# Kernel optimization log

Hardware: AMD Instinct MI355X
Metric: run time of the kernel (lower is better)

Reference implementation:

```python
import jax, jax.numpy as jnp
import numpy as np

D_MODEL = 1024
N_HEADS = 16
D_HEAD = 64


def setup_inputs() -> dict:
    key = jax.random.key(0)
    ks = jax.random.split(key, 5)
    B, T = 2, 2048
    scale = 1.0 / np.sqrt(D_MODEL)
    x = jax.random.normal(ks[0], (B, T, D_MODEL), dtype=jnp.float32)
    Wq = jax.random.normal(ks[1], (N_HEADS * D_HEAD, D_MODEL), dtype=jnp.float32) * scale
    Wk = jax.random.normal(ks[2], (N_HEADS * D_HEAD, D_MODEL), dtype=jnp.float32) * scale
    Wv = jax.random.normal(ks[3], (N_HEADS * D_HEAD, D_MODEL), dtype=jnp.float32) * scale
    Wo = jax.random.normal(ks[4], (D_MODEL, N_HEADS * D_HEAD), dtype=jnp.float32) * scale
    return {"x": x, "Wq": Wq, "Wk": Wk, "Wv": Wv, "Wo": Wo}


def reference(x, Wq, Wk, Wv, Wo):
    B, T, D = x.shape
    # Linear(y = x @ W.T), then split heads: [B, H, T, d]
    def split_heads(y):
        return y.reshape(B, T, N_HEADS, D_HEAD).transpose(0, 2, 1, 3)
    q = split_heads(x @ Wq.T)
    k = split_heads(x @ Wk.T)
    v = split_heads(x @ Wv.T)
    scale = D_HEAD ** -0.5
    # Materialized [B, H, T, T] scores, as in the original module
    scores = jnp.einsum('bhtd,bhTd->bhtT', q, k) * scale
    attn = jax.nn.softmax(scores, axis=-1)
    y = jnp.einsum('bhtT,bhTd->bhtd', attn, v)
    y = y.transpose(0, 2, 1, 3).reshape(B, T, N_HEADS * D_HEAD)
    return y @ Wo.T
```

## Files before the change

kernel.cpp:

```cpp
#include <hip/hip_runtime.h>
#include <hip/hip_bf16.h>

typedef __attribute__((ext_vector_type(8))) short bf16x8;
typedef __attribute__((ext_vector_type(8))) unsigned short u16x8;
typedef __attribute__((ext_vector_type(4))) float f32x4;
typedef unsigned short u16t;

#define DEVINL static __device__ __forceinline__

DEVINL u16t f2bf(float f) {
  union { __hip_bfloat16 h; u16t u; } cv;
  cv.h = __float2bfloat16(f);
  return cv.u;
}

DEVINL unsigned cvt_pk_bf16(float a, float b) {
  unsigned r;
  asm("v_cvt_pk_bf16_f32 %0, %1, %2" : "=v"(r) : "v"(a), "v"(b));
  return r;
}

DEVINL void async16(void* lds, const void* g) {
  __builtin_amdgcn_global_load_lds((const __attribute__((address_space(1))) void*)g,
                                   (__attribute__((address_space(3))) void*)lds,
                                   16, 0, 0);
}

__global__ __launch_bounds__(256) void convert_bf16(
    const float* __restrict__ x,  const float* __restrict__ wq,
    const float* __restrict__ wk, const float* __restrict__ wv,
    const float* __restrict__ wo,
    u16t* __restrict__ xb, u16t* __restrict__ wqb, u16t* __restrict__ wob) {
  const int blk = blockIdx.x;
  const int tid = threadIdx.x;
  if (blk < 896) {
    const int lane = tid & 63, w = tid >> 6;
    const int r = lane & 15, cw = lane >> 4;
    int mg, half, row0;
    const float* src; u16t* dst;
    if (blk < 512) { mg = blk >> 1; half = blk & 1; src = x; dst = xb; row0 = mg * 16; }
    else {
      const int wblk = blk - 512;
      mg = wblk >> 1; half = wblk & 1; dst = wqb;
      const int n0 = mg * 16;
      if (n0 < 1024)      { src = wq; row0 = n0; }
      else if (n0 < 2048) { src = wk; row0 = n0 - 1024; }
      else                { src = wv; row0 = n0 - 2048; }
    }
    #pragma unroll
    for (int ic = 0; ic < 4; ++ic) {
      const int c2 = half * 64 + w * 16 + ic * 4 + cw;
      const float4 v0 = *(const float4*)&src[(size_t)(row0 + r) * 1024 + c2 * 8];
      const float4 v1 = *(const float4*)&src[(size_t)(row0 + r) * 1024 + c2 * 8 + 4];
      u16x8 o;
      o[0] = f2bf(v0.x); o[1] = f2bf(v0.y); o[2] = f2bf(v0.z); o[3] = f2bf(v0.w);
      o[4] = f2bf(v1.x); o[5] = f2bf(v1.y); o[6] = f2bf(v1.z); o[7] = f2bf(v1.w);
      *(u16x8*)&dst[((size_t)mg * 128 + c2) * 128 + r * 8] = o;
    }
  } else {
    const int row = blk - 896;
    const size_t i = (size_t)row * 1024 + (size_t)tid * 4;
    const float4 v = *(const float4*)&wo[i];
    ushort4 rr;
    rr.x = f2bf(v.x); rr.y = f2bf(v.y); rr.z = f2bf(v.z); rr.w = f2bf(v.w);
    *(ushort4*)&wob[i] = rr;
  }
}

__global__ __launch_bounds__(256, 3) void gemm_fs(
    const u16t* __restrict__ A, const u16t* __restrict__ B,
    void* __restrict__ C0, void* __restrict__ C1, void* __restrict__ C2) {
  const int tid = threadIdx.x;
  const int lane = tid & 63;
  const int w = tid >> 6;
  const int wm = w >> 1, wn = w & 1;
  const int quad = lane >> 4, cl = lane & 15;
  const int m0 = blockIdx.y * 128;
  const int n0 = blockIdx.x * 128;

  const u16t* Ap = A + ((size_t)((m0 >> 4) + wm * 4) * 128 + quad) * 128 + cl * 8;
  const u16t* Bp = B + ((size_t)((n0 >> 4) + wn * 4) * 128 + quad) * 128 + cl * 8;

  f32x4 acc[4][4] = {};
  bf16x8 afA[4], bfA[4], afB[4], bfB[4];

  #define LOADP(af_, bf_, kp_)                                                \
    {                                                                         \
      _Pragma("unroll")                                                       \
      for (int i = 0; i < 4; ++i)                                             \
        af_[i] = *(const bf16x8*)&Ap[(size_t)i * 16384 + (kp_) * 512];        \
      _Pragma("unroll")                                                       \
      for (int j = 0; j < 4; ++j)                                             \
        bf_[j] = *(const bf16x8*)&Bp[(size_t)j * 16384 + (kp_) * 512];        \
    }

  #define MFMAP(af_, bf_)                                                     \
    {                                                                         \
      _Pragma("unroll")                                                       \
      for (int i = 0; i < 4; ++i)                                             \
        _Pragma("unroll")                                                     \
        for (int j = 0; j < 4; ++j)                                           \
          acc[i][j] = __builtin_amdgcn_mfma_f32_16x16x32_bf16(af_[i], bf_[j], acc[i][j], 0, 0, 0); \
    }

  LOADP(afA, bfA, 0);
  __builtin_amdgcn_sched_barrier(0);
  #pragma unroll 1
  for (int kp = 0; kp < 32; kp += 2) {
    LOADP(afB, bfB, kp + 1);
    __builtin_amdgcn_sched_barrier(0);
    MFMAP(afA, bfA);
    if (kp + 2 < 32) LOADP(afA, bfA, kp + 2);
    __builtin_amdgcn_sched_barrier(0);
    MFMAP(afB, bfB);
  }
  #undef LOADP
  #undef MFMAP

  const int nz = n0 >> 10;
  #pragma unroll
  for (int i = 0; i < 4; ++i)
    #pragma unroll
    for (int j = 0; j < 4; ++j) {
      const int mb = m0 + wm * 64 + i * 16 + quad * 4;
      const int n  = n0 + wn * 64 + j * 16 + cl;
      const int nw = n & 1023, h = nw >> 6, d = nw & 63;
      const int b = mb >> 11, tb = mb & 2047;
      const size_t bh = (size_t)(b * 16 + h);
      if (nz == 2) {
        ushort4 v4;
        v4.x = f2bf(acc[i][j][0]); v4.y = f2bf(acc[i][j][1]);
        v4.z = f2bf(acc[i][j][2]); v4.w = f2bf(acc[i][j][3]);
        const size_t addr = (bh << 17) +
            (size_t)(((d >> 4) * 256 + (tb >> 3)) * 128 + (d & 15) * 8 + (tb & 7));
        *(ushort4*)&((u16t*)C2)[addr] = v4;
      } else if (nz == 1) {
        const size_t basea = (bh << 17) +
            (size_t)(((tb >> 4) * 8 + (d >> 3)) * 128 + (d & 7));
        #pragma unroll
        for (int r = 0; r < 4; ++r)
          ((u16t*)C1)[basea + ((tb & 15) + r) * 8] = f2bf(acc[i][j][r]);
      } else {
        #pragma unroll
        for (int r = 0; r < 4; ++r)
          ((u16t*)C0)[(bh * 2048 + tb + r) * 64 + d] =
              f2bf(acc[i][j][r] * 0.18033688011112043f);
      }
    }
}

template <int MODE, int BM>
__global__ __launch_bounds__(256) void gemm_bt(
    const u16t* __restrict__ A, const u16t* __restrict__ B,
    void* __restrict__ C0, void* __restrict__ C1, void* __restrict__ C2,
    int M, int N, int K) {
  constexpr int MI = BM / 32;
  __shared__ u16t As[2][BM * 32];
  __shared__ u16t Bs[2][128 * 32];

  const int tid = threadIdx.x;
  const int lane = tid & 63;
  const int w = tid >> 6;
  const int wm = w >> 1, wn = w & 1;
  const int quad = lane >> 4, cl = lane & 15;
  const int m0 = blockIdx.y * BM;
  const int n0 = blockIdx.x * 128;

  const int srow = lane >> 2;
  const int scol = (lane & 3) * 8;

  f32x4 acc[MI][4] = {};

  #define STAGEP(b, kp)                                                       \
    {                                                                         \
      _Pragma("unroll")                                                       \
      for (int ii = 0; ii < BM / 64; ++ii) {                                  \
        const int c = w + ii * 4;                                             \
        async16(&As[b][c * 512],                                              \
                &A[(size_t)(m0 + c * 16 + srow) * K + (kp) * 32 + scol]);     \
      }                                                                       \
      _Pragma("unroll")                                                       \
      for (int ii = 0; ii < 2; ++ii) {                                        \
        const int c = w + ii * 4;                                             \
        async16(&Bs[b][c * 512],                                              \
                &B[(size_t)(n0 + c * 16 + srow) * K + (kp) * 32 + scol]);     \
      }                                                                       \
    }

  #define COMPUTEP(b)                                                         \
    {                                                                         \
      bf16x8 af[MI], bfr[4];                                                  \
      _Pragma("unroll")                                                       \
      for (int i = 0; i < MI; ++i)                                            \
        af[i] = *(const bf16x8*)&As[b][(wm * (BM / 2) + i * 16 + cl) * 32 + quad * 8]; \
      _Pragma("unroll")                                                       \
      for (int j = 0; j < 4; ++j)                                             \
        bfr[j] = *(const bf16x8*)&Bs[b][(wn * 64 + j * 16 + cl) * 32 + quad * 8]; \
      _Pragma("unroll")                                                       \
      for (int i = 0; i < MI; ++i)                                            \
        _Pragma("unroll")                                                     \
        for (int j = 0; j < 4; ++j)                                           \
          acc[i][j] = __builtin_amdgcn_mfma_f32_16x16x32_bf16(af[i], bfr[j], acc[i][j], 0, 0, 0); \
    }

  const int NP = K >> 5;
  STAGEP(0, 0);
  __syncthreads();
  for (int kp = 0; kp < NP; kp += 2) {
    if (kp + 1 < NP) STAGEP(1, kp + 1);
    COMPUTEP(0);
    __syncthreads();
    if (kp + 2 < NP) STAGEP(0, kp + 2);
    COMPUTEP(1);
    __syncthreads();
  }
  #undef STAGEP
  #undef COMPUTEP

  #pragma unroll
  for (int i = 0; i < MI; ++i)
    #pragma unroll
    for (int j = 0; j < 4; ++j) {
      const int mb = m0 + wm * (BM / 2) + i * 16 + quad * 4;
      const int n  = n0 + wn * 64 + j * 16 + cl;
      if (MODE == 0) {
        #pragma unroll
        for (int r = 0; r < 4; ++r)
          ((float*)C0)[(size_t)(mb + r) * N + n] = acc[i][j][r];
      }
      (void)C1; (void)C2;
    }
}

__global__ __launch_bounds__(256, 2) void flash_attn(
    const u16t* __restrict__ Q, const u16t* __restrict__ Kt,
    const u16t* __restrict__ Vt, u16t* __restrict__ Y) {
  __shared__ u16t Ps[4 * 32 * 136];
  const int tid = threadIdx.x;
  const int lane = tid & 63;
  const int w = tid >> 6;
  const int quad = lane >> 4, cl = lane & 15;
  const int bh = blockIdx.x;
  const int q0 = blockIdx.y * 128 + w * 32;
  const u16t* Kb = Kt + ((size_t)bh << 17);
  const u16t* Vb = Vt + ((size_t)bh << 17);

  bf16x8 aq[2][2];
  #pragma unroll
  for (int h = 0; h < 2; ++h)
    #pragma unroll
    for (int ks = 0; ks < 2; ++ks)
      aq[h][ks] = *(const bf16x8*)&Q[((size_t)bh * 2048 + q0 + 16 * h + cl) * 64 + ks * 32 + quad * 8];

  bf16x8 ones8;
  #pragma unroll
  for (int i = 0; i < 8; ++i) ones8[i] = (short)0x3F80;

  f32x4 o[2][4] = {};
  f32x4 psum[2] = {};

  u16t* Pw = &Ps[w * 32 * 136];

  for (int jt = 0; jt < 16; ++jt) {
    const int j0 = jt * 128;

    bf16x8 kf[2][8];
    #pragma unroll
    for (int ks = 0; ks < 2; ++ks)
      #pragma unroll
      for (int js = 0; js < 8; ++js)
        kf[ks][js] = *(const bf16x8*)&Kb[(size_t)((((j0 >> 4) + js) * 8 + ks * 4) * 128) + lane * 8];
    __builtin_amdgcn_sched_barrier(0);

    f32x4 s0[8] = {}, s1[8] = {};
    __builtin_amdgcn_s_setprio(1);
    #pragma unroll
    for (int ks = 0; ks < 2; ++ks) {
      #pragma unroll
      for (int js = 0; js < 8; ++js)
        s0[js] = __builtin_amdgcn_mfma_f32_16x16x32_bf16(kf[ks][js], aq[0][ks], s0[js], 0, 0, 0);
      #pragma unroll
      for (int js = 0; js < 8; ++js)
        s1[js] = __builtin_amdgcn_mfma_f32_16x16x32_bf16(kf[ks][js], aq[1][ks], s1[js], 0, 0, 0);
    }
    __builtin_amdgcn_s_setprio(0);

    bf16x8 vf[4][4];
    #pragma unroll
    for (int ks = 0; ks < 4; ++ks)
      #pragma unroll
      for (int ds = 0; ds < 4; ++ds)
        vf[ks][ds] = *(const bf16x8*)&Vb[(size_t)((ds * 256 + (j0 >> 3) + ks * 4) * 128) + lane * 8];
    __builtin_amdgcn_sched_barrier(0);

    #pragma unroll
    for (int js = 0; js < 8; ++js) {
      uint2 pk0, pk1;
      pk0.x = cvt_pk_bf16(__builtin_exp2f(s0[js][0]), __builtin_exp2f(s0[js][1]));
      pk0.y = cvt_pk_bf16(__builtin_exp2f(s0[js][2]), __builtin_exp2f(s0[js][3]));
      *(uint2*)&Pw[cl * 136 + js * 16 + quad * 4] = pk0;
      pk1.x = cvt_pk_bf16(__builtin_exp2f(s1[js][0]), __builtin_exp2f(s1[js][1]));
      pk1.y = cvt_pk_bf16(__builtin_exp2f(s1[js][2]), __builtin_exp2f(s1[js][3]));
      *(uint2*)&Pw[(16 + cl) * 136 + js * 16 + quad * 4] = pk1;
    }

    __builtin_amdgcn_s_setprio(1);
    #pragma unroll
    for (int ks = 0; ks < 4; ++ks) {
      const bf16x8 ap0 = *(const bf16x8*)&Pw[cl * 136 + ks * 32 + quad * 8];
      const bf16x8 ap1 = *(const bf16x8*)&Pw[(16 + cl) * 136 + ks * 32 + quad * 8];
      psum[0] = __builtin_amdgcn_mfma_f32_16x16x32_bf16(ap0, ones8, psum[0], 0, 0, 0);
      psum[1] = __builtin_amdgcn_mfma_f32_16x16x32_bf16(ap1, ones8, psum[1], 0, 0, 0);
      #pragma unroll
      for (int ds = 0; ds < 4; ++ds) {
        o[0][ds] = __builtin_amdgcn_mfma_f32_16x16x32_bf16(ap0, vf[ks][ds], o[0][ds], 0, 0, 0);
        o[1][ds] = __builtin_amdgcn_mfma_f32_16x16x32_bf16(ap1, vf[ks][ds], o[1][ds], 0, 0, 0);
      }
    }
    __builtin_amdgcn_s_setprio(0);
  }

  const int b = bh >> 4, hd = bh & 15;
  #pragma unroll
  for (int h = 0; h < 2; ++h) {
    float inv[4];
    #pragma unroll
    for (int r = 0; r < 4; ++r) inv[r] = __builtin_amdgcn_rcpf(psum[h][r]);
    #pragma unroll
    for (int ds = 0; ds < 4; ++ds)
      #pragma unroll
      for (int r = 0; r < 4; ++r) {
        const int t = q0 + 16 * h + quad * 4 + r;
        const int d = ds * 16 + cl;
        Y[((size_t)b * 2048 + t) * 1024 + hd * 64 + d] = f2bf(o[h][ds][r] * inv[r]);
      }
  }
}

extern "C" void kernel_launch(void* const* d_in, const int* in_sizes, int n_in,
                              void* d_out, int out_size, void* d_ws, size_t ws_size,
                              hipStream_t stream) {
  (void)in_sizes; (void)n_in; (void)out_size; (void)ws_size;
  const float* x  = (const float*)d_in[0];
  const float* Wq = (const float*)d_in[1];
  const float* Wk = (const float*)d_in[2];
  const float* Wv = (const float*)d_in[3];
  const float* Wo = (const float*)d_in[4];

  char* ws = (char*)d_ws;
  const size_t MB = 1024 * 1024;
  u16t* xb  = (u16t*)(ws);
  u16t* Wqb = (u16t*)(ws + 8 * MB);
  u16t* Wob = (u16t*)(ws + 14 * MB);
  u16t* Qw  = (u16t*)(ws + 16 * MB);
  u16t* Ktw = (u16t*)(ws + 24 * MB);
  u16t* Vtw = (u16t*)(ws + 32 * MB);
  u16t* Yw  = xb;

  convert_bf16<<<1920, 256, 0, stream>>>(x, Wq, Wk, Wv, Wo, xb, Wqb, Wob);
  gemm_fs<<<dim3(24, 32), 256, 0, stream>>>(xb, Wqb, Qw, Ktw, Vtw);
  flash_attn<<<dim3(32, 16), 256, 0, stream>>>(Qw, Ktw, Vtw, Yw);
  gemm_bt<0, 64><<<dim3(8, 64), 256, 0, stream>>>(
      Yw, Wob, d_out, d_out, d_out, 4096, 1024, 1024);
}
```

Baseline: 189.3 us.

## Use pre-swizzled fragment layout for output projection, drop LDS-staged GEMM

The attention kernel now writes Y directly in the fragment-tiled layout that gemm_fs reads. Wo is converted into the same tiled layout. The output projection then runs through the register-direct gemm_fs template (MI=2) in place of the LDS-staged gemm_bt. This removes the LDS staging and barriers from the final GEMM. The cost is scattered 2-byte stores from attention and loads that are no longer shared within a block.

```diff
diff --git a/kernel.cpp b/kernel.cpp
--- a/kernel.cpp
+++ b/kernel.cpp
@@ -18,12 +18,6 @@
   unsigned r;
   asm("v_cvt_pk_bf16_f32 %0, %1, %2" : "=v"(r) : "v"(a), "v"(b));
   return r;
-}
-
-DEVINL void async16(void* lds, const void* g) {
-  __builtin_amdgcn_global_load_lds((const __attribute__((address_space(1))) void*)g,
-                                   (__attribute__((address_space(3))) void*)lds,
-                                   16, 0, 0);
 }
 
 __global__ __launch_bounds__(256) void convert_bf16(
@@ -33,40 +27,36 @@
     u16t* __restrict__ xb, u16t* __restrict__ wqb, u16t* __restrict__ wob) {
   const int blk = blockIdx.x;
   const int tid = threadIdx.x;
-  if (blk < 896) {
-    const int lane = tid & 63, w = tid >> 6;
-    const int r = lane & 15, cw = lane >> 4;
-    int mg, half, row0;
-    const float* src; u16t* dst;
-    if (blk < 512) { mg = blk >> 1; half = blk & 1; src = x; dst = xb; row0 = mg * 16; }
-    else {
-      const int wblk = blk - 512;
-      mg = wblk >> 1; half = wblk & 1; dst = wqb;
-      const int n0 = mg * 16;
-      if (n0 < 1024)      { src = wq; row0 = n0; }
-      else if (n0 < 2048) { src = wk; row0 = n0 - 1024; }
-      else                { src = wv; row0 = n0 - 2048; }
-    }
-    #pragma unroll
-    for (int ic = 0; ic < 4; ++ic) {
-      const int c2 = half * 64 + w * 16 + ic * 4 + cw;
-      const float4 v0 = *(const float4*)&src[(size_t)(row0 + r) * 1024 + c2 * 8];
-      const float4 v1 = *(const float4*)&src[(size_t)(row0 + r) * 1024 + c2 * 8 + 4];
-      u16x8 o;
-      o[0] = f2bf(v0.x); o[1] = f2bf(v0.y); o[2] = f2bf(v0.z); o[3] = f2bf(v0.w);
-      o[4] = f2bf(v1.x); o[5] = f2bf(v1.y); o[6] = f2bf(v1.z); o[7] = f2bf(v1.w);
-      *(u16x8*)&dst[((size_t)mg * 128 + c2) * 128 + r * 8] = o;
-    }
+  const int lane = tid & 63, w = tid >> 6;
+  const int r = lane & 15, cw = lane >> 4;
+  int mg, half, row0;
+  const float* src; u16t* dst;
+  if (blk < 512) {
+    mg = blk >> 1; half = blk & 1; src = x; dst = xb; row0 = mg * 16;
+  } else if (blk < 896) {
+    const int wblk = blk - 512;
+    mg = wblk >> 1; half = wblk & 1; dst = wqb;
+    const int n0 = mg * 16;
+    if (n0 < 1024)      { src = wq; row0 = n0; }
+    else if (n0 < 2048) { src = wk; row0 = n0 - 1024; }
+    else                { src = wv; row0 = n0 - 2048; }
   } else {
-    const int row = blk - 896;
-    const size_t i = (size_t)row * 1024 + (size_t)tid * 4;
-    const float4 v = *(const float4*)&wo[i];
-    ushort4 rr;
-    rr.x = f2bf(v.x); rr.y = f2bf(v.y); rr.z = f2bf(v.z); rr.w = f2bf(v.w);
-    *(ushort4*)&wob[i] = rr;
-  }
-}
-
+    const int oblk = blk - 896;
+    mg = oblk >> 1; half = oblk & 1; src = wo; dst = wob; row0 = mg * 16;
+  }
+  #pragma unroll
+  for (int ic = 0; ic < 4; ++ic) {
+    const int c2 = half * 64 + w * 16 + ic * 4 + cw;
+    const float4 v0 = *(const float4*)&src[(size_t)(row0 + r) * 1024 + c2 * 8];
+    const float4 v1 = *(const float4*)&src[(size_t)(row0 + r) * 1024 + c2 * 8 + 4];
+    u16x8 o;
+    o[0] = f2bf(v0.x); o[1] = f2bf(v0.y); o[2] = f2bf(v0.z); o[3] = f2bf(v0.w);
+    o[4] = f2bf(v1.x); o[5] = f2bf(v1.y); o[6] = f2bf(v1.z); o[7] = f2bf(v1.w);
+    *(u16x8*)&dst[((size_t)mg * 128 + c2) * 128 + r * 8] = o;
+  }
+}
+
+template <int MODE, int MI>
 __global__ __launch_bounds__(256, 3) void gemm_fs(
     const u16t* __restrict__ A, const u16t* __restrict__ B,
     void* __restrict__ C0, void* __restrict__ C1, void* __restrict__ C2) {
@@ -75,19 +65,19 @@
   const int w = tid >> 6;
   const int wm = w >> 1, wn = w & 1;
   const int quad = lane >> 4, cl = lane & 15;
-  const int m0 = blockIdx.y * 128;
+  const int m0 = blockIdx.y * (MI * 32);
   const int n0 = blockIdx.x * 128;
 
-  const u16t* Ap = A + ((size_t)((m0 >> 4) + wm * 4) * 128 + quad) * 128 + cl * 8;
+  const u16t* Ap = A + ((size_t)((m0 >> 4) + wm * MI) * 128 + quad) * 128 + cl * 8;
   const u16t* Bp = B + ((size_t)((n0 >> 4) + wn * 4) * 128 + quad) * 128 + cl * 8;
 
-  f32x4 acc[4][4] = {};
-  bf16x8 afA[4], bfA[4], afB[4], bfB[4];
+  f32x4 acc[MI][4] = {};
+  bf16x8 afA[MI], bfA[4], afB[MI], bfB[4];
 
   #define LOADP(af_, bf_, kp_)                                                \
     {                                                                         \
       _Pragma("unroll")                                                       \
-      for (int i = 0; i < 4; ++i)                                             \
+      for (int i = 0; i < MI; ++i)                                            \
         af_[i] = *(const bf16x8*)&Ap[(size_t)i * 16384 + (kp_) * 512];        \
       _Pragma("unroll")                                                       \
       for (int j = 0; j < 4; ++j)                                             \
@@ -97,7 +87,7 @@
   #define MFMAP(af_, bf_)                                                     \
     {                                                                         \
       _Pragma("unroll")                                                       \
-      for (int i = 0; i < 4; ++i)                                             \
+      for (int i = 0; i < MI; ++i)                                            \
         _Pragma("unroll")                                                     \
         for (int j = 0; j < 4; ++j)                                           \
           acc[i][j] = __builtin_amdgcn_mfma_f32_16x16x32_bf16(af_[i], bf_[j], acc[i][j], 0, 0, 0); \
@@ -119,116 +109,39 @@
 
   const int nz = n0 >> 10;
   #pragma unroll
-  for (int i = 0; i < 4; ++i)
+  for (int i = 0; i < MI; ++i)
     #pragma unroll
     for (int j = 0; j < 4; ++j) {
-      const int mb = m0 + wm * 64 + i * 16 + quad * 4;
-      const int n  = n0 + wn * 64 + j * 16 + cl;
-      const int nw = n & 1023, h = nw >> 6, d = nw & 63;
-      const int b = mb >> 11, tb = mb & 2047;
-      const size_t bh = (size_t)(b * 16 + h);
-      if (nz == 2) {
-        ushort4 v4;
-        v4.x = f2bf(acc[i][j][0]); v4.y = f2bf(acc[i][j][1]);
-        v4.z = f2bf(acc[i][j][2]); v4.w = f2bf(acc[i][j][3]);
-        const size_t addr = (bh << 17) +
-            (size_t)(((d >> 4) * 256 + (tb >> 3)) * 128 + (d & 15) * 8 + (tb & 7));
-        *(ushort4*)&((u16t*)C2)[addr] = v4;
-      } else if (nz == 1) {
-        const size_t basea = (bh << 17) +
-            (size_t)(((tb >> 4) * 8 + (d >> 3)) * 128 + (d & 7));
-        #pragma unroll
-        for (int r = 0; r < 4; ++r)
-          ((u16t*)C1)[basea + ((tb & 15) + r) * 8] = f2bf(acc[i][j][r]);
-      } else {
-        #pragma unroll
-        for (int r = 0; r < 4; ++r)
-          ((u16t*)C0)[(bh * 2048 + tb + r) * 64 + d] =
-              f2bf(acc[i][j][r] * 0.18033688011112043f);
-      }
-    }
-}
-
-template <int MODE, int BM>
-__global__ __launch_bounds__(256) void gemm_bt(
-    const u16t* __restrict__ A, const u16t* __restrict__ B,
-    void* __restrict__ C0, void* __restrict__ C1, void* __restrict__ C2,
-    int M, int N, int K) {
-  constexpr int MI = BM / 32;
-  __shared__ u16t As[2][BM * 32];
-  __shared__ u16t Bs[2][128 * 32];
-
-  const int tid = threadIdx.x;
-  const int lane = tid & 63;
-  const int w = tid >> 6;
-  const int wm = w >> 1, wn = w & 1;
-  const int quad = lane >> 4, cl = lane & 15;
-  const int m0 = blockIdx.y * BM;
-  const int n0 = blockIdx.x * 128;
-
-  const int srow = lane >> 2;
-  const int scol = (lane & 3) * 8;
-
-  f32x4 acc[MI][4] = {};
-
-  #define STAGEP(b, kp)                                                       \
-    {                                                                         \
-      _Pragma("unroll")                                                       \
-      for (int ii = 0; ii < BM / 64; ++ii) {                                  \
-        const int c = w + ii * 4;                                             \
-        async16(&As[b][c * 512],                                              \
-                &A[(size_t)(m0 + c * 16 + srow) * K + (kp) * 32 + scol]);     \
-      }                                                                       \
-      _Pragma("unroll")                                                       \
-      for (int ii = 0; ii < 2; ++ii) {                                        \
-        const int c = w + ii * 4;                                             \
-        async16(&Bs[b][c * 512],                                              \
-                &B[(size_t)(n0 + c * 16 + srow) * K + (kp) * 32 + scol]);     \
-      }                                                                       \
-    }
-
-  #define COMPUTEP(b)                                                         \
-    {                                                                         \
-      bf16x8 af[MI], bfr[4];                                                  \
-      _Pragma("unroll")                                                       \
-      for (int i = 0; i < MI; ++i)                                            \
-        af[i] = *(const bf16x8*)&As[b][(wm * (BM / 2) + i * 16 + cl) * 32 + quad * 8]; \
-      _Pragma("unroll")                                                       \
-      for (int j = 0; j < 4; ++j)                                             \
-        bfr[j] = *(const bf16x8*)&Bs[b][(wn * 64 + j * 16 + cl) * 32 + quad * 8]; \
-      _Pragma("unroll")                                                       \
-      for (int i = 0; i < MI; ++i)                                            \
-        _Pragma("unroll")                                                     \
-        for (int j = 0; j < 4; ++j)                                           \
-          acc[i][j] = __builtin_amdgcn_mfma_f32_16x16x32_bf16(af[i], bfr[j], acc[i][j], 0, 0, 0); \
-    }
-
-  const int NP = K >> 5;
-  STAGEP(0, 0);
-  __syncthreads();
-  for (int kp = 0; kp < NP; kp += 2) {
-    if (kp + 1 < NP) STAGEP(1, kp + 1);
-    COMPUTEP(0);
-    __syncthreads();
-    if (kp + 2 < NP) STAGEP(0, kp + 2);
-    COMPUTEP(1);
-    __syncthreads();
-  }
-  #undef STAGEP
-  #undef COMPUTEP
-
-  #pragma unroll
-  for (int i = 0; i < MI; ++i)
-    #pragma unroll
-    for (int j = 0; j < 4; ++j) {
-      const int mb = m0 + wm * (BM / 2) + i * 16 + quad * 4;
+      const int mb = m0 + wm * (MI * 16) + i * 16 + quad * 4;
       const int n  = n0 + wn * 64 + j * 16 + cl;
       if (MODE == 0) {
         #pragma unroll
         for (int r = 0; r < 4; ++r)
-          ((float*)C0)[(size_t)(mb + r) * N + n] = acc[i][j][r];
+          ((float*)C0)[(size_t)(mb + r) * 1024 + n] = acc[i][j][r];
+      } else {
+        const int nw = n & 1023, h = nw >> 6, d = nw & 63;
+        const int b = mb >> 11, tb = mb & 2047;
+        const size_t bh = (size_t)(b * 16 + h);
+        if (nz == 2) {
+          ushort4 v4;
+          v4.x = f2bf(acc[i][j][0]); v4.y = f2bf(acc[i][j][1]);
+          v4.z = f2bf(acc[i][j][2]); v4.w = f2bf(acc[i][j][3]);
+          const size_t addr = (bh << 17) +
+              (size_t)(((d >> 4) * 256 + (tb >> 3)) * 128 + (d & 15) * 8 + (tb & 7));
+          *(ushort4*)&((u16t*)C2)[addr] = v4;
+        } else if (nz == 1) {
+          const size_t basea = (bh << 17) +
+              (size_t)(((tb >> 4) * 8 + (d >> 3)) * 128 + (d & 7));
+          #pragma unroll
+          for (int r = 0; r < 4; ++r)
+            ((u16t*)C1)[basea + ((tb & 15) + r) * 8] = f2bf(acc[i][j][r]);
+        } else {
+          #pragma unroll
+          for (int r = 0; r < 4; ++r)
+            ((u16t*)C0)[(bh * 2048 + tb + r) * 64 + d] =
+                f2bf(acc[i][j][r] * 0.18033688011112043f);
+        }
       }
-      (void)C1; (void)C2;
     }
 }
 
@@ -321,18 +234,20 @@
   }
 
   const int b = bh >> 4, hd = bh & 15;
+  const int mgbase = (b * 2048 + q0) >> 4;
   #pragma unroll
   for (int h = 0; h < 2; ++h) {
     float inv[4];
     #pragma unroll
     for (int r = 0; r < 4; ++r) inv[r] = __builtin_amdgcn_rcpf(psum[h][r]);
+    const size_t rowb = (size_t)((mgbase + h) * 128 + hd * 8) * 128;
     #pragma unroll
     for (int ds = 0; ds < 4; ++ds)
       #pragma unroll
       for (int r = 0; r < 4; ++r) {
-        const int t = q0 + 16 * h + quad * 4 + r;
-        const int d = ds * 16 + cl;
-        Y[((size_t)b * 2048 + t) * 1024 + hd * 64 + d] = f2bf(o[h][ds][r] * inv[r]);
+        const size_t addr = rowb + (size_t)(ds * 2 + (cl >> 3)) * 128 +
+                            (quad * 4 + r) * 8 + (cl & 7);
+        Y[addr] = f2bf(o[h][ds][r] * inv[r]);
       }
   }
 }
@@ -357,9 +272,9 @@
   u16t* Vtw = (u16t*)(ws + 32 * MB);
   u16t* Yw  = xb;
 
-  convert_bf16<<<1920, 256, 0, stream>>>(x, Wq, Wk, Wv, Wo, xb, Wqb, Wob);
-  gemm_fs<<<dim3(24, 32), 256, 0, stream>>>(xb, Wqb, Qw, Ktw, Vtw);
+  convert_bf16<<<1024, 256, 0, stream>>>(x, Wq, Wk, Wv, Wo, xb, Wqb, Wob);
+  gemm_fs<1, 4><<<dim3(24, 32), 256, 0, stream>>>(xb, Wqb, Qw, Ktw, Vtw);
   flash_attn<<<dim3(32, 16), 256, 0, stream>>>(Qw, Ktw, Vtw, Yw);
-  gemm_bt<0, 64><<<dim3(8, 64), 256, 0, stream>>>(
-      Yw, Wob, d_out, d_out, d_out, 4096, 1024, 1024);
-}
+  gemm_fs<0, 2><<<dim3(8, 64), 256, 0, stream>>>(
+      Yw, Wob, d_out, d_out, d_out);
+}
```

Result: faster. 183.9 us (-2.9%).
